# Optimization experiments

Hardware: AMD Instinct MI355X
Metric: run time of the kernel (lower is better)

## Reference

```python
import jax, jax.numpy as jnp
import numpy as np

# DoG parameters derived from init kwargs: sigma_low=1.0, truncate=4.0
SIGMA_LOW = 1.0
SIGMA_HIGH = 1.6  # sigma_low * 1.6
KSIZE_LOW = 9     # 2*ceil(4.0*1.0)+1
KSIZE_HIGH = 15   # 2*ceil(4.0*1.6)+1


def gaussian_kernel1d(ksize: int, sigma: float) -> jnp.ndarray:
    # Matches kornia's 1D gaussian: centered, normalized to sum 1.
    t = jnp.arange(ksize, dtype=jnp.float32) - (ksize - 1) / 2.0
    g = jnp.exp(-(t * t) / (2.0 * sigma * sigma))
    return g / jnp.sum(g)


def _conv1d_along_axis(x: jnp.ndarray, g: jnp.ndarray, axis: int) -> jnp.ndarray:
    # x: (B, C, D, H, W); depthwise 1D cross-correlation along `axis` with
    # replicate ('edge') boundary handling, as in kornia filter3d(border_type='replicate').
    C = x.shape[1]
    k = g.shape[0]
    pads = [(0, 0)] * 5
    pads[axis] = (k // 2, k // 2)
    xp = jnp.pad(x, pads, mode='edge')
    kshape = [1, 1, 1]
    kshape[axis - 2] = k
    w = jnp.tile(g.reshape(1, 1, *kshape), (C, 1, 1, 1, 1))  # (C,1,kd,kh,kw)
    return jax.lax.conv_general_dilated(
        xp, w, window_strides=(1, 1, 1), padding='VALID',
        dimension_numbers=('NCDHW', 'OIDHW', 'NCDHW'),
        feature_group_count=C)


def gaussian_blur3d(x: jnp.ndarray, sigma: float, ksize: int) -> jnp.ndarray:
    # The 3D kernel is an outer product of normalized 1D gaussians, so the
    # dense 3D convolution is exactly equal to three separable 1D passes.
    g = gaussian_kernel1d(ksize, sigma)
    for ax in (2, 3, 4):
        x = _conv1d_along_axis(x, g, ax)
    return x


def setup_inputs() -> dict:
    key = jax.random.key(0)
    x = jax.random.normal(key, (2, 1, 160, 160, 160), dtype=jnp.float32)
    return {"x": x}


def reference(x) -> jnp.ndarray:
    low_pass = gaussian_blur3d(x, SIGMA_LOW, KSIZE_LOW)
    high_pass = gaussian_blur3d(x, SIGMA_HIGH, KSIZE_HIGH)
    return low_pass - high_pass
```

## Files before the change

kernel.cpp:

```cpp
#include <hip/hip_runtime.h>
#include <math.h>

#define DIMS 160
#define PLANE (DIMS*DIMS)
#define VOL (DIMS*PLANE)
#define NB 2
#define RH 7
#define RL 4
#define KH 15
#define KL 9

struct DoGW { float gl[KL]; float gh[KH]; };


#define A_TS 32
#define A_RR 46
#define A_SRAW 48
#define A_SH 50
#define A_SL 42

__global__ __launch_bounds__(256, 4)
void dog_xy(const float* __restrict__ X, float* __restrict__ wsH,
            float* __restrict__ wsL, DoGW w) {
  __shared__ __align__(16) float sRaw[A_RR * A_SRAW];
  __shared__ __align__(16) float sHx[A_TS * A_SH];
  __shared__ __align__(16) float sLx[A_TS * A_SL];

  const int bid = blockIdx.x;
  const int xt = bid % 5, yt = (bid / 5) % 5, zp = bid / 25;
  const int x0 = xt * A_TS, y0 = yt * A_TS;
  const float* P = X + (size_t)zp * PLANE;
  const int tid = threadIdx.x;
  const bool xin = (xt > 0) && (xt < 4);

  #pragma unroll
  for (int rr = 0; rr < 3; ++rr) {
    const int u = tid + rr * 256;
    if (u < A_RR * 12) {
      const int row = u / 12, q = u % 12;
      const int yg = min(max(y0 + row - RH, 0), DIMS - 1);
      const float* rp = P + (size_t)yg * DIMS;
      const int gx = x0 - 8 + 4 * q;
      float4 v;
      if (xin || (gx >= 0 && gx + 4 <= DIMS)) {
        v = *(const float4*)(rp + gx);
      } else {
        v.x = rp[min(max(gx + 0, 0), DIMS - 1)];
        v.y = rp[min(max(gx + 1, 0), DIMS - 1)];
        v.z = rp[min(max(gx + 2, 0), DIMS - 1)];
        v.w = rp[min(max(gx + 3, 0), DIMS - 1)];
      }
      *(float4*)&sRaw[row * A_SRAW + 4 * q] = v;
    }
  }
  __syncthreads();

  #pragma unroll
  for (int rr = 0; rr < 2; ++rr) {
    const int u = tid + rr * 256;
    if (u < A_RR * 8) {
      const int row = u >> 3, q = u & 7;
      const float* p = &sRaw[row * A_SRAW + 4 * q];
      float v[20];
      #pragma unroll
      for (int j = 0; j < 5; ++j) {
        float4 t = *(const float4*)(p + 4 * j);
        v[4*j] = t.x; v[4*j+1] = t.y; v[4*j+2] = t.z; v[4*j+3] = t.w;
      }
      #pragma unroll
      for (int c = 0; c < 4; ++c) {
        float a = 0.f;
        #pragma unroll
        for (int k = 0; k < KH; ++k) a = fmaf(w.gh[k], v[c + 1 + k], a);
        sHx[(4 * q + c) * A_SH + row] = a;
      }
      if (row >= 3 && row <= 42) {
        #pragma unroll
        for (int c = 0; c < 4; ++c) {
          float a = 0.f;
          #pragma unroll
          for (int k = 0; k < KL; ++k) a = fmaf(w.gl[k], v[c + 4 + k], a);
          sLx[(4 * q + c) * A_SL + (row - 3)] = a;
        }
      }
    }
  }
  __syncthreads();

  float* const oH = wsH + (size_t)zp * PLANE;
  float* const oL = wsL + (size_t)zp * PLANE;
  #pragma unroll
  for (int rr = 0; rr < 2; ++rr) {
    const int u = tid + rr * 256;
    const int cx = u & 31, cy0 = 2 * ((u >> 5) & 15);
    float f[16], g[10];
    #pragma unroll
    for (int j = 0; j < 8; ++j) {
      float2 t = *(const float2*)&sHx[cx * A_SH + cy0 + 2 * j];
      f[2*j] = t.x; f[2*j+1] = t.y;
    }
    #pragma unroll
    for (int j = 0; j < 5; ++j) {
      float2 t = *(const float2*)&sLx[cx * A_SL + cy0 + 2 * j];
      g[2*j] = t.x; g[2*j+1] = t.y;
    }
    float ph0 = 0.f, ph1 = 0.f, pl0 = 0.f, pl1 = 0.f;
    #pragma unroll
    for (int j = 0; j < KH; ++j) {
      ph0 = fmaf(w.gh[j], f[j], ph0);
      ph1 = fmaf(w.gh[j], f[j + 1], ph1);
    }
    #pragma unroll
    for (int j = 0; j < KL; ++j) {
      pl0 = fmaf(w.gl[j], g[j], pl0);
      pl1 = fmaf(w.gl[j], g[j + 1], pl1);
    }
    const int o = (y0 + cy0) * DIMS + x0 + cx;
    oH[o] = ph0; oH[o + DIMS] = ph1;
    oL[o] = pl0; oL[o + DIMS] = pl1;
  }
}

#define B_CZ 40
#define B_NP (B_CZ + 2*RH)

__global__ __launch_bounds__(256, 4)
void dog_z(const float* __restrict__ wsH, const float* __restrict__ wsL,
           float* __restrict__ out, DoGW w) {
  const int bid = blockIdx.x;
  const int cb = bid % 200, zc = bid / 200;
  const int col = cb * 256 + threadIdx.x;
  const int b = col / PLANE, rem = col % PLANE;
  const int zb = zc * B_CZ;
  const float* __restrict__ pH = wsH + (size_t)b * VOL + rem;
  const float* __restrict__ pL = wsL + (size_t)b * VOL + rem;
  float* __restrict__ po = out + (size_t)b * VOL + rem;

  auto ldH = [&](int q) -> float {
    const int zs = min(max(zb - RH + q, 0), DIMS - 1);
    return pH[(size_t)zs * PLANE];
  };
  auto ldL = [&](int q) -> float {
    const int zs = min(max(zb - RH + q, 0), DIMS - 1);
    return pL[(size_t)zs * PLANE];
  };

  float D[KH];
  #pragma unroll
  for (int i = 0; i < KH; ++i) D[i] = 0.f;

  float hA = ldH(0), lA = ldL(0);
  float hB = ldH(1), lB = ldL(1);
  #pragma unroll 6
  for (int q = 0; q < B_NP; ++q) {
    float hC = 0.f, lC = 0.f;
    if (q + 2 < B_NP) { hC = ldH(q + 2); lC = ldL(q + 2); }
    #pragma unroll
    for (int i = 0; i < KH; ++i) D[i] = fmaf(-w.gh[KH - 1 - i], hA, D[i]);
    #pragma unroll
    for (int i = 3; i < KL + 3; ++i) D[i] = fmaf(w.gl[KL + 2 - i], lA, D[i]);
    if (q >= 2 * RH) po[(size_t)(zb + q - 2 * RH) * PLANE] = D[0];
    #pragma unroll
    for (int i = 0; i < KH - 1; ++i) D[i] = D[i + 1];
    D[KH - 1] = 0.f;
    hA = hB; lA = lB; hB = hC; lB = lC;
  }
}

#define TSX 16
#define TSY 32
#define NTX (DIMS/TSX)
#define NTY (DIMS/TSY)
#define CZ 32
#define NCH (DIMS/CZ)
#define NSTEPS (CZ + 2*RH)
#define YHR (TSY + 2*RH)
#define SR 48
#define SH 50
#define SL 42
#define RAWSZ (YHR*SR)
#define XHSZ (TSX*SH)
#define XLSZ (TSX*SL)
#define NBLK (NTX*NTY*NCH*NB)

__global__ __launch_bounds__(512, 4)
void dog_fb(const float* __restrict__ X, float* __restrict__ out, DoGW w) {
  __shared__ __align__(16) float sRaw[2][RAWSZ];
  __shared__ __align__(16) float sXh[2][XHSZ];
  __shared__ __align__(16) float sXl[2][XLSZ];

  const int bid = blockIdx.x;
  const int xt = bid % NTX;
  const int yt = (bid / NTX) % NTY;
  const int zc = (bid / (NTX * NTY)) % NCH;
  const int b  = bid / (NTX * NTY * NCH);
  const int x0 = xt * TSX, y0 = yt * TSY, z0 = zc * CZ;
  const float* Xb = X + (size_t)b * VOL;
  const int tid = threadIdx.x;
  const bool xfast = (x0 >= 8) && (x0 + 24 <= DIMS);

  const bool y_on = tid < 256;
  const int cx  = tid & 15;
  const int cy0 = 2 * ((tid >> 4) & 15);
  const int hb = cx * SH + cy0;
  const int lb = cx * SL + cy0;
  float* const obase = out + (size_t)b * VOL + (size_t)(y0 + cy0) * DIMS + (x0 + cx);

  const bool x_on = (tid >= 256) && (tid < 256 + YHR * 4);
  const int xu = tid - 256;
  const int xr = xu >> 2, xq = xu & 3;

  const bool l_on = tid >= (512 - YHR * 4);
  const int lu = tid - (512 - YHR * 4);
  const int lrow = lu >> 2, lt = lu & 3;
  const int lyg = min(max(y0 + lrow - RH, 0), DIMS - 1);
  const int lxb = x0 - 8 + 4 * lt;

  float4 vA, vB;
  auto loadP = [&](int s) {
    const int zsrc = min(max(z0 - RH + s, 0), DIMS - 1);
    const float* rowp = Xb + ((size_t)zsrc * DIMS + lyg) * DIMS;
    if (xfast) {
      vA = *(const float4*)(rowp + lxb);
      vB = *(const float4*)(rowp + lxb + 16);
    } else {
      vA.x = rowp[min(max(lxb + 0, 0), DIMS - 1)];
      vA.y = rowp[min(max(lxb + 1, 0), DIMS - 1)];
      vA.z = rowp[min(max(lxb + 2, 0), DIMS - 1)];
      vA.w = rowp[min(max(lxb + 3, 0), DIMS - 1)];
      vB.x = rowp[min(max(lxb + 16, 0), DIMS - 1)];
      vB.y = rowp[min(max(lxb + 17, 0), DIMS - 1)];
      vB.z = rowp[min(max(lxb + 18, 0), DIMS - 1)];
      vB.w = rowp[min(max(lxb + 19, 0), DIMS - 1)];
    }
  };
  auto stageP = [&](int buf) {
    float* p = &sRaw[buf][lrow * SR + 4 * lt];
    *(float4*)(p) = vA;
    *(float4*)(p + 16) = vB;
  };

  float D0[KH], D1[KH];
  #pragma unroll
  for (int i = 0; i < KH; ++i) { D0[i] = 0.f; D1[i] = 0.f; }

  auto consumeQ = [&](int q) {
    const int qb = q & 1;
    float f[16], g[10];
    #pragma unroll
    for (int j = 0; j < 8; ++j) {
      float2 t = *(const float2*)&sXh[qb][hb + 2 * j];
      f[2 * j] = t.x; f[2 * j + 1] = t.y;
    }
    #pragma unroll
    for (int j = 0; j < 5; ++j) {
      float2 t = *(const float2*)&sXl[qb][lb + 2 * j];
      g[2 * j] = t.x; g[2 * j + 1] = t.y;
    }
    float ph0 = 0.f, ph1 = 0.f, pl0 = 0.f, pl1 = 0.f;
    #pragma unroll
    for (int j = 0; j < KH; ++j) {
      ph0 = fmaf(w.gh[j], f[j], ph0);
      ph1 = fmaf(w.gh[j], f[j + 1], ph1);
    }
    #pragma unroll
    for (int j = 0; j < KL; ++j) {
      pl0 = fmaf(w.gl[j], g[j], pl0);
      pl1 = fmaf(w.gl[j], g[j + 1], pl1);
    }
    #pragma unroll
    for (int i = 0; i < KH; ++i) {
      D0[i] = fmaf(-w.gh[KH - 1 - i], ph0, D0[i]);
      D1[i] = fmaf(-w.gh[KH - 1 - i], ph1, D1[i]);
    }
    #pragma unroll
    for (int i = 3; i < KL + 3; ++i) {
      D0[i] = fmaf(w.gl[KL + 2 - i], pl0, D0[i]);
      D1[i] = fmaf(w.gl[KL + 2 - i], pl1, D1[i]);
    }
    if (q >= 2 * RH) {
      float* op = obase + (size_t)(z0 + q - 2 * RH) * PLANE;
      op[0]    = D0[0];
      op[DIMS] = D1[0];
    }
    #pragma unroll
    for (int i = 0; i < KH - 1; ++i) { D0[i] = D0[i + 1]; D1[i] = D1[i + 1]; }
    D0[KH - 1] = 0.f; D1[KH - 1] = 0.f;
  };

  auto xconvP = [&](int cur) {
    const float* p = &sRaw[cur][xr * SR + 4 * xq];
    float v[20];
    #pragma unroll
    for (int j = 0; j < 5; ++j) {
      float4 t = *(const float4*)(p + 4 * j);
      v[4 * j] = t.x; v[4 * j + 1] = t.y; v[4 * j + 2] = t.z; v[4 * j + 3] = t.w;
    }
    #pragma unroll
    for (int c = 0; c < 4; ++c) {
      float a = 0.f;
      #pragma unroll
      for (int k = 0; k < KH; ++k) a = fmaf(w.gh[k], v[c + 1 + k], a);
      sXh[cur][(4 * xq + c) * SH + xr] = a;
    }
    if (xr >= 3 && xr <= 42) {
      #pragma unroll
      for (int c = 0; c < 4; ++c) {
        float a = 0.f;
        #pragma unroll
        for (int k = 0; k < KL; ++k) a = fmaf(w.gl[k], v[c + 4 + k], a);
        sXl[cur][(4 * xq + c) * SL + (xr - 3)] = a;
      }
    }
  };

  if (l_on) { loadP(0); stageP(0); loadP(1); }
  __syncthreads();

  #pragma unroll 5
  for (int s = 0; s < NSTEPS; ++s) {
    const int cur = s & 1;
    if (l_on) {
      if (s + 1 < NSTEPS) stageP(1 - cur);
      if (s + 2 < NSTEPS) loadP(s + 2);
    }
    if (y_on && s >= 1) consumeQ(s - 1);
    if (x_on) xconvP(cur);
    __syncthreads();
  }
  if (y_on) consumeQ(NSTEPS - 1);
}

extern "C" void kernel_launch(void* const* d_in, const int* in_sizes, int n_in,
                              void* d_out, int out_size, void* d_ws, size_t ws_size,
                              hipStream_t stream) {
  const float* X = (const float*)d_in[0];
  float* out = (float*)d_out;

  DoGW w;
  {
    double s = 0.0;
    for (int i = 0; i < KL; ++i) {
      double t = i - (KL - 1) / 2.0;
      double g = exp(-(t * t) / (2.0 * 1.0 * 1.0));
      w.gl[i] = (float)g; s += g;
    }
    for (int i = 0; i < KL; ++i) w.gl[i] = (float)((double)w.gl[i] / s);
    s = 0.0;
    for (int i = 0; i < KH; ++i) {
      double t = i - (KH - 1) / 2.0;
      double g = exp(-(t * t) / (2.0 * 1.6 * 1.6));
      w.gh[i] = (float)g; s += g;
    }
    for (int i = 0; i < KH; ++i) w.gh[i] = (float)((double)w.gh[i] / s);
  }

  const size_t need = 2ull * NB * VOL * sizeof(float);
  if (ws_size >= need) {
    float* wsH = (float*)d_ws;
    float* wsL = wsH + (size_t)NB * VOL;
    dog_xy<<<NB * DIMS * 25, 256, 0, stream>>>(X, wsH, wsL, w);
    dog_z<<<(NB * PLANE / 256) * (DIMS / B_CZ), 256, 0, stream>>>(wsH, wsL, out, w);
  } else {
    dog_fb<<<NBLK, 512, 0, stream>>>(X, out, w);
  }
}
```

Before: 124.0 us.

## Interleave H/L intermediates as float2, load raw rows directly, halve z-chunk

```diff
diff --git a/kernel.cpp b/kernel.cpp
--- a/kernel.cpp
+++ b/kernel.cpp
@@ -15,14 +15,11 @@
 
 #define A_TS 32
 #define A_RR 46
-#define A_SRAW 48
 #define A_SH 50
 #define A_SL 42
 
 __global__ __launch_bounds__(256, 4)
-void dog_xy(const float* __restrict__ X, float* __restrict__ wsH,
-            float* __restrict__ wsL, DoGW w) {
-  __shared__ __align__(16) float sRaw[A_RR * A_SRAW];
+void dog_xy(const float* __restrict__ X, float2* __restrict__ wsI, DoGW w) {
   __shared__ __align__(16) float sHx[A_TS * A_SH];
   __shared__ __align__(16) float sLx[A_TS * A_SL];
 
@@ -34,37 +31,26 @@
   const bool xin = (xt > 0) && (xt < 4);
 
   #pragma unroll
-  for (int rr = 0; rr < 3; ++rr) {
-    const int u = tid + rr * 256;
-    if (u < A_RR * 12) {
-      const int row = u / 12, q = u % 12;
-      const int yg = min(max(y0 + row - RH, 0), DIMS - 1);
-      const float* rp = P + (size_t)yg * DIMS;
-      const int gx = x0 - 8 + 4 * q;
-      float4 v;
-      if (xin || (gx >= 0 && gx + 4 <= DIMS)) {
-        v = *(const float4*)(rp + gx);
-      } else {
-        v.x = rp[min(max(gx + 0, 0), DIMS - 1)];
-        v.y = rp[min(max(gx + 1, 0), DIMS - 1)];
-        v.z = rp[min(max(gx + 2, 0), DIMS - 1)];
-        v.w = rp[min(max(gx + 3, 0), DIMS - 1)];
-      }
-      *(float4*)&sRaw[row * A_SRAW + 4 * q] = v;
-    }
-  }
-  __syncthreads();
-
-  #pragma unroll
   for (int rr = 0; rr < 2; ++rr) {
     const int u = tid + rr * 256;
     if (u < A_RR * 8) {
       const int row = u >> 3, q = u & 7;
-      const float* p = &sRaw[row * A_SRAW + 4 * q];
+      const int yg = min(max(y0 + row - RH, 0), DIMS - 1);
+      const float* rp = P + (size_t)yg * DIMS;
+      const int gx0 = x0 - 8 + 4 * q;
       float v[20];
       #pragma unroll
       for (int j = 0; j < 5; ++j) {
-        float4 t = *(const float4*)(p + 4 * j);
+        const int gx = gx0 + 4 * j;
+        float4 t;
+        if (xin || (gx >= 0 && gx + 4 <= DIMS)) {
+          t = *(const float4*)(rp + gx);
+        } else {
+          t.x = rp[min(max(gx + 0, 0), DIMS - 1)];
+          t.y = rp[min(max(gx + 1, 0), DIMS - 1)];
+          t.z = rp[min(max(gx + 2, 0), DIMS - 1)];
+          t.w = rp[min(max(gx + 3, 0), DIMS - 1)];
+        }
         v[4*j] = t.x; v[4*j+1] = t.y; v[4*j+2] = t.z; v[4*j+3] = t.w;
       }
       #pragma unroll
@@ -87,83 +73,67 @@
   }
   __syncthreads();
 
-  float* const oH = wsH + (size_t)zp * PLANE;
-  float* const oL = wsL + (size_t)zp * PLANE;
-  #pragma unroll
-  for (int rr = 0; rr < 2; ++rr) {
-    const int u = tid + rr * 256;
-    const int cx = u & 31, cy0 = 2 * ((u >> 5) & 15);
-    float f[16], g[10];
-    #pragma unroll
-    for (int j = 0; j < 8; ++j) {
+  {
+    const int cx = tid & 31, cy0 = 4 * (tid >> 5);
+    float f[18], g[12];
+    #pragma unroll
+    for (int j = 0; j < 9; ++j) {
       float2 t = *(const float2*)&sHx[cx * A_SH + cy0 + 2 * j];
       f[2*j] = t.x; f[2*j+1] = t.y;
     }
     #pragma unroll
-    for (int j = 0; j < 5; ++j) {
+    for (int j = 0; j < 6; ++j) {
       float2 t = *(const float2*)&sLx[cx * A_SL + cy0 + 2 * j];
       g[2*j] = t.x; g[2*j+1] = t.y;
     }
-    float ph0 = 0.f, ph1 = 0.f, pl0 = 0.f, pl1 = 0.f;
-    #pragma unroll
-    for (int j = 0; j < KH; ++j) {
-      ph0 = fmaf(w.gh[j], f[j], ph0);
-      ph1 = fmaf(w.gh[j], f[j + 1], ph1);
-    }
-    #pragma unroll
-    for (int j = 0; j < KL; ++j) {
-      pl0 = fmaf(w.gl[j], g[j], pl0);
-      pl1 = fmaf(w.gl[j], g[j + 1], pl1);
-    }
-    const int o = (y0 + cy0) * DIMS + x0 + cx;
-    oH[o] = ph0; oH[o + DIMS] = ph1;
-    oL[o] = pl0; oL[o + DIMS] = pl1;
+    float2* const o = wsI + (size_t)zp * PLANE + (size_t)(y0 + cy0) * DIMS + (x0 + cx);
+    #pragma unroll
+    for (int c = 0; c < 4; ++c) {
+      float ph = 0.f, pl = 0.f;
+      #pragma unroll
+      for (int j = 0; j < KH; ++j) ph = fmaf(w.gh[j], f[c + j], ph);
+      #pragma unroll
+      for (int j = 0; j < KL; ++j) pl = fmaf(w.gl[j], g[c + j], pl);
+      o[(size_t)c * DIMS] = make_float2(ph, pl);
+    }
   }
 }
 
-#define B_CZ 40
+#define B_CZ 20
 #define B_NP (B_CZ + 2*RH)
 
 __global__ __launch_bounds__(256, 4)
-void dog_z(const float* __restrict__ wsH, const float* __restrict__ wsL,
-           float* __restrict__ out, DoGW w) {
+void dog_z(const float2* __restrict__ wsI, float* __restrict__ out, DoGW w) {
   const int bid = blockIdx.x;
   const int cb = bid % 200, zc = bid / 200;
   const int col = cb * 256 + threadIdx.x;
   const int b = col / PLANE, rem = col % PLANE;
   const int zb = zc * B_CZ;
-  const float* __restrict__ pH = wsH + (size_t)b * VOL + rem;
-  const float* __restrict__ pL = wsL + (size_t)b * VOL + rem;
+  const float2* __restrict__ pI = wsI + (size_t)b * VOL + rem;
   float* __restrict__ po = out + (size_t)b * VOL + rem;
 
-  auto ldH = [&](int q) -> float {
+  auto ld = [&](int q) -> float2 {
     const int zs = min(max(zb - RH + q, 0), DIMS - 1);
-    return pH[(size_t)zs * PLANE];
-  };
-  auto ldL = [&](int q) -> float {
-    const int zs = min(max(zb - RH + q, 0), DIMS - 1);
-    return pL[(size_t)zs * PLANE];
+    return pI[(size_t)zs * PLANE];
   };
 
   float D[KH];
   #pragma unroll
   for (int i = 0; i < KH; ++i) D[i] = 0.f;
 
-  float hA = ldH(0), lA = ldL(0);
-  float hB = ldH(1), lB = ldL(1);
-  #pragma unroll 6
+  float2 vA = ld(0), vB = ld(1);
+  #pragma unroll
   for (int q = 0; q < B_NP; ++q) {
-    float hC = 0.f, lC = 0.f;
-    if (q + 2 < B_NP) { hC = ldH(q + 2); lC = ldL(q + 2); }
-    #pragma unroll
-    for (int i = 0; i < KH; ++i) D[i] = fmaf(-w.gh[KH - 1 - i], hA, D[i]);
-    #pragma unroll
-    for (int i = 3; i < KL + 3; ++i) D[i] = fmaf(w.gl[KL + 2 - i], lA, D[i]);
+    float2 vC = (q + 2 < B_NP) ? ld(q + 2) : make_float2(0.f, 0.f);
+    #pragma unroll
+    for (int i = 0; i < KH; ++i) D[i] = fmaf(-w.gh[KH - 1 - i], vA.x, D[i]);
+    #pragma unroll
+    for (int i = 3; i < KL + 3; ++i) D[i] = fmaf(w.gl[KL + 2 - i], vA.y, D[i]);
     if (q >= 2 * RH) po[(size_t)(zb + q - 2 * RH) * PLANE] = D[0];
     #pragma unroll
     for (int i = 0; i < KH - 1; ++i) D[i] = D[i + 1];
     D[KH - 1] = 0.f;
-    hA = hB; lA = lB; hB = hC; lB = lC;
+    vA = vB; vB = vC;
   }
 }
 
@@ -355,12 +325,11 @@
     for (int i = 0; i < KH; ++i) w.gh[i] = (float)((double)w.gh[i] / s);
   }
 
-  const size_t need = 2ull * NB * VOL * sizeof(float);
+  const size_t need = (size_t)NB * VOL * sizeof(float2);
   if (ws_size >= need) {
-    float* wsH = (float*)d_ws;
-    float* wsL = wsH + (size_t)NB * VOL;
-    dog_xy<<<NB * DIMS * 25, 256, 0, stream>>>(X, wsH, wsL, w);
-    dog_z<<<(NB * PLANE / 256) * (DIMS / B_CZ), 256, 0, stream>>>(wsH, wsL, out, w);
+    float2* wsI = (float2*)d_ws;
+    dog_xy<<<NB * DIMS * 25, 256, 0, stream>>>(X, wsI, w);
+    dog_z<<<200 * (DIMS / B_CZ), 256, 0, stream>>>(wsI, out, w);
   } else {
     dog_fb<<<NBLK, 512, 0, stream>>>(X, out, w);
   }
```

Result: slower. 138.7 us (+11.9%).
